# Kernel tuning notes

Measured on AMD Instinct MI355X. Metric: run time of the kernel, lower is better.

## Reference

```python
import jax, jax.numpy as jnp
import numpy as np

N_NODES = 50000
N_EDGES = 800000
H = 64      # node_hidden_size
S = 16      # static_feature_size
EF = 16     # edge_feature_size
ATT_IN = 2 * H + 2 * S + EF   # 176
ATT_W = 2 * H + EF            # 144
UPD_IN = 2 * H                # 128
UPD_W = 2 * H                 # 128


def setup_inputs() -> dict:
    key = jax.random.key(0)
    ks = jax.random.split(key, 12)
    x = jax.random.normal(ks[0], (N_NODES, H), dtype=jnp.float32)
    x_s = jax.random.normal(ks[1], (N_NODES, S), dtype=jnp.float32)
    edge_index = jax.random.randint(ks[2], (2, N_EDGES), 0, N_NODES, dtype=jnp.int32)
    edge_features = jax.random.normal(ks[3], (N_EDGES, EF), dtype=jnp.float32)

    def lin(k, out_dim, in_dim):
        lim = 1.0 / np.sqrt(in_dim)
        kw, kb = jax.random.split(k)
        W = jax.random.uniform(kw, (out_dim, in_dim), minval=-lim, maxval=lim, dtype=jnp.float32)
        b = jax.random.uniform(kb, (out_dim,), minval=-lim, maxval=lim, dtype=jnp.float32)
        return W, b

    att_w1, att_b1 = lin(ks[4], ATT_W, ATT_IN)
    att_w2, att_b2 = lin(ks[5], 1, ATT_W)
    upd_w1, upd_b1 = lin(ks[6], UPD_W, UPD_IN)
    upd_w2, upd_b2 = lin(ks[7], H, UPD_W)

    return {
        "x": x, "x_s": x_s, "edge_index": edge_index, "edge_features": edge_features,
        "att_w1": att_w1, "att_b1": att_b1, "att_w2": att_w2, "att_b2": att_b2,
        "upd_w1": upd_w1, "upd_b1": upd_b1, "upd_w2": upd_w2, "upd_b2": upd_b2,
    }


def segment_softmax(scores, segment_ids, num_segments):
    max_scores = jax.ops.segment_max(scores, segment_ids, num_segments=num_segments)
    exp_scores = jnp.exp(scores - max_scores[segment_ids])
    sum_exp = jax.ops.segment_sum(exp_scores, segment_ids, num_segments=num_segments)
    return exp_scores / (sum_exp[segment_ids] + 1e-9)


def reference(x, x_s, edge_index, edge_features,
              att_w1, att_b1, att_w2, att_b2,
              upd_w1, upd_b1, upd_w2, upd_b2):
    num_nodes = x.shape[0]
    src, dst = edge_index[0], edge_index[1]

    # gather per-edge features: [E, 2H+2S+EF]
    att_in = jnp.concatenate(
        [x[src], x[dst], x_s[src], x_s[dst], edge_features], axis=-1)

    # attention MLP (depth=1, relu hidden), squeeze to [E]
    h = jax.nn.relu(att_in @ att_w1.T + att_b1)
    raw = (h @ att_w2.T + att_b2).squeeze(-1)
    raw = jax.nn.leaky_relu(raw)

    attn = segment_softmax(raw, dst, num_nodes)

    # weighted scatter-sum of source hidden feats -> [N, H]
    aggregated = jax.ops.segment_sum(x[src] * attn[:, None], dst, num_segments=num_nodes)

    upd_in = jnp.concatenate([x, aggregated], axis=-1)
    u = jax.nn.relu(upd_in @ upd_w1.T + upd_b1)
    out = u @ upd_w2.T + upd_b2
    return jax.nn.relu(out)
```

## Files before the change

kernel.cpp:

```cpp
#include <hip/hip_runtime.h>
#include <math.h>

#define N_NODES_C 50000
#define E_C       800000
#define ATT_IN_C  176
#define ATT_HID_C 144
#define SCAN_B    98
#define UPD_TILES 3125
#define DEG_B     3125
#define CVT_B     1978
#define SCORE_B   256

typedef __attribute__((ext_vector_type(8))) __bf16 bf16x8;
typedef __attribute__((ext_vector_type(4))) float f32x4;

#define O_RAW   0L
#define O_DEG   3200000L
#define O_OFF   3400704L
#define O_CUR   3601408L
#define O_CSR   3802112L
#define O_EFC   7002112L
#define O_XB    32602112L
#define O_XSB   39002112L
#define O_W1B   40602112L
#define O_UW1B  40653312L
#define O_UW2B  40686080L
#define O_AGGB  40702464L
#define O_PSUM  O_AGGB

__device__ __forceinline__ bf16x8 bzero8() {
    bf16x8 z;
#pragma unroll
    for (int i = 0; i < 8; ++i) z[i] = (__bf16)0.0f;
    return z;
}

__global__ __launch_bounds__(256) void k_prep(
    const int* __restrict__ ei,
    const float* __restrict__ x, const float* __restrict__ xs,
    const float* __restrict__ w1,
    const float* __restrict__ uw1, const float* __restrict__ uw2,
    int* __restrict__ deg,
    __bf16* __restrict__ xb, __bf16* __restrict__ xsb,
    __bf16* __restrict__ w1b,
    __bf16* __restrict__ uw1b, __bf16* __restrict__ uw2b)
{
    int bid = blockIdx.x;
    if (bid < DEG_B) {
        int e = bid * 256 + threadIdx.x;
        if (e < E_C) atomicAdd(&deg[ei[E_C + e]], 1);
        return;
    }
    long g = (long)(bid - DEG_B) * 256 + threadIdx.x;
    const long G_X = 400000, G_XS = 500000, G_W1 = 503168,
               G_UW1 = 505216, G_UW2 = 506240;
    if (g >= G_UW2) return;
    const float* src; __bf16* dst; long off;
    if (g < G_X)        { src = x;   dst = xb;   off = g * 8; }
    else if (g < G_XS)  { src = xs;  dst = xsb;  off = (g - G_X) * 8; }
    else if (g < G_W1)  { src = w1;  dst = w1b;  off = (g - G_XS) * 8; }
    else if (g < G_UW1) { src = uw1; dst = uw1b; off = (g - G_W1) * 8; }
    else                { src = uw2; dst = uw2b; off = (g - G_UW1) * 8; }
    float4 a = *(const float4*)(src + off);
    float4 b = *(const float4*)(src + off + 4);
    bf16x8 o;
    o[0] = (__bf16)a.x; o[1] = (__bf16)a.y; o[2] = (__bf16)a.z; o[3] = (__bf16)a.w;
    o[4] = (__bf16)b.x; o[5] = (__bf16)b.y; o[6] = (__bf16)b.z; o[7] = (__bf16)b.w;
    *(bf16x8*)(dst + off) = o;
}

__global__ __launch_bounds__(256) void k_scan1(const int* __restrict__ deg,
                                               int* __restrict__ psum) {
    __shared__ int red[256];
    int b = blockIdx.x, t = threadIdx.x;
    int i = b * 512 + t * 2;
    int s = 0;
    if (i < N_NODES_C) s += deg[i];
    if (i + 1 < N_NODES_C) s += deg[i + 1];
    red[t] = s;
    __syncthreads();
#pragma unroll
    for (int off = 128; off > 0; off >>= 1) {
        if (t < off) red[t] += red[t + off];
        __syncthreads();
    }
    if (t == 0) psum[b] = red[0];
}

__global__ __launch_bounds__(256) void k_scan3(const int* __restrict__ deg,
                                               const int* __restrict__ psum,
                                               int* __restrict__ offsets,
                                               int* __restrict__ cursor) {
    __shared__ int sc[256];
    __shared__ int bo[2];
    int b = blockIdx.x, t = threadIdx.x;
    if (t < 64) {
        int v1 = (t < SCAN_B) ? psum[t] : 0;
        int v2 = (t + 64 < SCAN_B) ? psum[t + 64] : 0;
        int c   = ((t < b) ? v1 : 0) + ((t + 64 < b) ? v2 : 0);
        int tot = v1 + v2;
#pragma unroll
        for (int off = 32; off > 0; off >>= 1) {
            c   += __shfl_xor(c, off, 64);
            tot += __shfl_xor(tot, off, 64);
        }
        if (t == 0) { bo[0] = c; bo[1] = tot; }
    }
    int i = b * 512 + t * 2;
    int d0 = (i < N_NODES_C) ? deg[i] : 0;
    int d1 = (i + 1 < N_NODES_C) ? deg[i + 1] : 0;
    int s = d0 + d1;
    sc[t] = s;
    __syncthreads();
#pragma unroll
    for (int off = 1; off < 256; off <<= 1) {
        int val = sc[t];
        int add = (t >= off) ? sc[t - off] : 0;
        __syncthreads();
        sc[t] = val + add;
        __syncthreads();
    }
    int excl = bo[0] + sc[t] - s;
    if (i < N_NODES_C)     { offsets[i]     = excl;      cursor[i]     = excl; }
    if (i + 1 < N_NODES_C) { offsets[i + 1] = excl + d0; cursor[i + 1] = excl + d0; }
    if (b == 0 && t == 0)  offsets[N_NODES_C] = bo[1];
}

__global__ __launch_bounds__(256) void k_fill(const int* __restrict__ ei,
                                              const float* __restrict__ ef,
                                              int* __restrict__ cursor,
                                              unsigned* __restrict__ csrp,
                                              __bf16* __restrict__ efc) {
    int e = blockIdx.x * blockDim.x + threadIdx.x;
    if (e < E_C) {
        int src  = ei[e];
        int dst  = ei[E_C + e];
        int slot = atomicAdd(&cursor[dst], 1);
        csrp[slot] = (unsigned)src | ((unsigned)dst << 16);
        const float4* efp = (const float4*)(ef + (long)e * 16);
        float4 f0 = efp[0], f1 = efp[1], f2 = efp[2], f3 = efp[3];
        bf16x8 o0, o1;
        o0[0] = (__bf16)f0.x; o0[1] = (__bf16)f0.y; o0[2] = (__bf16)f0.z; o0[3] = (__bf16)f0.w;
        o0[4] = (__bf16)f1.x; o0[5] = (__bf16)f1.y; o0[6] = (__bf16)f1.z; o0[7] = (__bf16)f1.w;
        o1[0] = (__bf16)f2.x; o1[1] = (__bf16)f2.y; o1[2] = (__bf16)f2.z; o1[3] = (__bf16)f2.w;
        o1[4] = (__bf16)f3.x; o1[5] = (__bf16)f3.y; o1[6] = (__bf16)f3.z; o1[7] = (__bf16)f3.w;
        __bf16* d = efc + (long)slot * 16;
        *(bf16x8*)d       = o0;
        *(bf16x8*)(d + 8) = o1;
    }
}

__device__ __forceinline__ void load_afrags(
    int src, int dst, long slot, int quad,
    const __bf16* __restrict__ xb, const __bf16* __restrict__ xsb,
    const __bf16* __restrict__ efc,
    bf16x8 a[6])
{
    const __bf16* px = xb + (long)src * 64 + quad * 8;
    const __bf16* pd = xb + (long)dst * 64 + quad * 8;
    a[0] = *(const bf16x8*)(px);
    a[1] = *(const bf16x8*)(px + 32);
    a[2] = *(const bf16x8*)(pd);
    a[3] = *(const bf16x8*)(pd + 32);
    if (quad < 2) {
        a[4] = *(const bf16x8*)(xsb + (long)src * 16 + quad * 8);
        a[5] = *(const bf16x8*)(efc + slot * 16 + quad * 8);
    } else {
        a[4] = *(const bf16x8*)(xsb + (long)dst * 16 + (quad - 2) * 8);
        a[5] = bzero8();
    }
}

__global__ __launch_bounds__(256) void k_scores_mfma(
    const __bf16* __restrict__ xb, const __bf16* __restrict__ xsb,
    const __bf16* __restrict__ efc, const __bf16* __restrict__ w1b,
    const unsigned* __restrict__ csrp,
    const float* __restrict__ b1, const float* __restrict__ w2,
    const float* __restrict__ b2, float* __restrict__ raw)
{
    __shared__ __bf16 w1s[144 * 184];
    int tid  = threadIdx.x;
    int lane = tid & 63;

    for (int c = tid; c < 144 * 22; c += 256) {
        int n = c / 22, kk = (c % 22) * 8;
        *(bf16x8*)&w1s[n * 184 + kk] = *(const bf16x8*)(w1b + (long)n * ATT_IN_C + kk);
    }
    for (int n = tid; n < 144; n += 256)
        *(bf16x8*)&w1s[n * 184 + 176] = bzero8();
    __syncthreads();

    int w = blockIdx.x * 4 + (tid >> 6);
    const int NP = E_C / 32;
    int per = (NP + 1023) / 1024;
    long j0 = (long)w * per;
    long j1 = j0 + per; if (j1 > NP) j1 = NP;
    if (j0 >= j1) return;

    int mrow = lane & 15;
    int quad = lane >> 4;
    const __bf16* wls = &w1s[mrow * 184 + quad * 8];

    float b1v[9], w2v[9];
#pragma unroll
    for (int nt = 0; nt < 9; ++nt) {
        int n = nt * 16 + mrow;
        b1v[nt] = b1[n];
        w2v[nt] = w2[n];
    }
    float b2v = b2[0];

    bf16x8 A0[6], B0[6], A1[6], B1[6];
    {
        unsigned e0 = csrp[j0 * 32 + mrow];
        unsigned e1 = csrp[j0 * 32 + 16 + mrow];
        load_afrags((int)(e0 & 0xFFFFu), (int)(e0 >> 16), j0 * 32 + mrow,
                    quad, xb, xsb, efc, A0);
        load_afrags((int)(e1 & 0xFFFFu), (int)(e1 >> 16), j0 * 32 + 16 + mrow,
                    quad, xb, xsb, efc, B0);
        if (j0 + 1 < j1) {
            unsigned f0 = csrp[(j0 + 1) * 32 + mrow];
            unsigned f1 = csrp[(j0 + 1) * 32 + 16 + mrow];
            load_afrags((int)(f0 & 0xFFFFu), (int)(f0 >> 16), (j0 + 1) * 32 + mrow,
                        quad, xb, xsb, efc, A1);
            load_afrags((int)(f1 & 0xFFFFu), (int)(f1 >> 16), (j0 + 1) * 32 + 16 + mrow,
                        quad, xb, xsb, efc, B1);
        }
    }

    auto body = [&](long j, bf16x8 (&FA)[6], bf16x8 (&FB)[6]) {
        unsigned u0 = 0, u1 = 0;
        bool rl = (j + 2 < j1);
        if (rl) {
            u0 = csrp[(j + 2) * 32 + mrow];
            u1 = csrp[(j + 2) * 32 + 16 + mrow];
        }

        f32x4 accA[9], accB[9];
#pragma unroll
        for (int nt = 0; nt < 9; ++nt) {
            accA[nt] = (f32x4){0.f, 0.f, 0.f, 0.f};
            accB[nt] = (f32x4){0.f, 0.f, 0.f, 0.f};
        }
#pragma unroll
        for (int ks = 0; ks < 6; ++ks) {
#pragma unroll
            for (int nt = 0; nt < 9; ++nt) {
                bf16x8 bf = *(const bf16x8*)(wls + nt * (16 * 184) + ks * 32);
                accA[nt] = __builtin_amdgcn_mfma_f32_16x16x32_bf16(
                    FA[ks], bf, accA[nt], 0, 0, 0);
                accB[nt] = __builtin_amdgcn_mfma_f32_16x16x32_bf16(
                    FB[ks], bf, accB[nt], 0, 0, 0);
            }
        }

        if (rl) {
            load_afrags((int)(u0 & 0xFFFFu), (int)(u0 >> 16), (j + 2) * 32 + mrow,
                        quad, xb, xsb, efc, FA);
            load_afrags((int)(u1 & 0xFFFFu), (int)(u1 >> 16), (j + 2) * 32 + 16 + mrow,
                        quad, xb, xsb, efc, FB);
        }

        float pA0 = 0.f, pA1 = 0.f, pA2 = 0.f, pA3 = 0.f;
        float pB0 = 0.f, pB1 = 0.f, pB2 = 0.f, pB3 = 0.f;
#pragma unroll
        for (int nt = 0; nt < 9; ++nt) {
            pA0 += w2v[nt] * fmaxf(accA[nt][0] + b1v[nt], 0.f);
            pA1 += w2v[nt] * fmaxf(accA[nt][1] + b1v[nt], 0.f);
            pA2 += w2v[nt] * fmaxf(accA[nt][2] + b1v[nt], 0.f);
            pA3 += w2v[nt] * fmaxf(accA[nt][3] + b1v[nt], 0.f);
            pB0 += w2v[nt] * fmaxf(accB[nt][0] + b1v[nt], 0.f);
            pB1 += w2v[nt] * fmaxf(accB[nt][1] + b1v[nt], 0.f);
            pB2 += w2v[nt] * fmaxf(accB[nt][2] + b1v[nt], 0.f);
            pB3 += w2v[nt] * fmaxf(accB[nt][3] + b1v[nt], 0.f);
        }
#pragma unroll
        for (int off = 1; off < 16; off <<= 1) {
            pA0 += __shfl_xor(pA0, off, 64);
            pA1 += __shfl_xor(pA1, off, 64);
            pA2 += __shfl_xor(pA2, off, 64);
            pA3 += __shfl_xor(pA3, off, 64);
            pB0 += __shfl_xor(pB0, off, 64);
            pB1 += __shfl_xor(pB1, off, 64);
            pB2 += __shfl_xor(pB2, off, 64);
            pB3 += __shfl_xor(pB3, off, 64);
        }
        if (mrow < 4) {
            float vA = (mrow == 0) ? pA0 : (mrow == 1) ? pA1 : (mrow == 2) ? pA2 : pA3;
            float vB = (mrow == 0) ? pB0 : (mrow == 1) ? pB1 : (mrow == 2) ? pB2 : pB3;
            vA += b2v; vB += b2v;
            vA = (vA >= 0.f) ? vA : 0.01f * vA;
            vB = (vB >= 0.f) ? vB : 0.01f * vB;
            raw[(j * 2) * 16 + quad * 4 + mrow]     = vA;
            raw[(j * 2 + 1) * 16 + quad * 4 + mrow] = vB;
        }
    };

    long j = j0;
    for (; j + 1 < j1; j += 2) {
        body(j,     A0, B0);
        body(j + 1, A1, B1);
    }
    if (j < j1) body(j, A0, B0);
}

__global__ __launch_bounds__(256) void k_agg(
    const __bf16* __restrict__ xb, const int* __restrict__ offsets,
    const unsigned* __restrict__ csrp,
    const float* __restrict__ raw, __bf16* __restrict__ aggb)
{
    int tid = threadIdx.x;
    int wave = tid >> 6, lane = tid & 63;
    int v = blockIdx.x * 4 + wave;
    if (v >= N_NODES_C) return;
    int s0 = offsets[v], s1 = offsets[v + 1];

    float m = -INFINITY;
    for (int p = s0 + lane; p < s1; p += 64) m = fmaxf(m, raw[p]);
#pragma unroll
    for (int off = 32; off > 0; off >>= 1) m = fmaxf(m, __shfl_xor(m, off, 64));

    float acc = 0.f, sum = 0.f;
    int p = s0;
    for (; p + 4 <= s1; p += 4) {
        unsigned c0 = csrp[p], c1 = csrp[p + 1], c2 = csrp[p + 2], c3 = csrp[p + 3];
        float r0 = raw[p], r1 = raw[p + 1], r2 = raw[p + 2], r3 = raw[p + 3];
        float v0 = (float)xb[(long)(c0 & 0xFFFFu) * 64 + lane];
        float v1 = (float)xb[(long)(c1 & 0xFFFFu) * 64 + lane];
        float v2 = (float)xb[(long)(c2 & 0xFFFFu) * 64 + lane];
        float v3 = (float)xb[(long)(c3 & 0xFFFFu) * 64 + lane];
        float w0 = expf(r0 - m), w1 = expf(r1 - m);
        float w2 = expf(r2 - m), w3 = expf(r3 - m);
        sum += (w0 + w1) + (w2 + w3);
        acc += w0 * v0 + w1 * v1 + w2 * v2 + w3 * v3;
    }
    for (; p < s1; ++p) {
        int src = (int)(csrp[p] & 0xFFFFu);
        float w = expf(raw[p] - m);
        sum += w;
        acc += w * (float)xb[(long)src * 64 + lane];
    }
    aggb[(long)v * 64 + lane] = (__bf16)(acc / (sum + 1e-9f));
}

__global__ __launch_bounds__(256) void k_upd_mfma(
    const __bf16* __restrict__ xb, const __bf16* __restrict__ aggb,
    const __bf16* __restrict__ w1b, const float* __restrict__ b1,
    const __bf16* __restrict__ w2b, const float* __restrict__ b2,
    float* __restrict__ out)
{
    __shared__ __bf16 ubuf[4][16 * 136];
    int tid = threadIdx.x, wid = tid >> 6, lane = tid & 63;
    int tile = blockIdx.x * 4 + wid;
    if (tile >= UPD_TILES) return;
    int mrow = lane & 15, quad = lane >> 4;

    long node = (long)tile * 16 + mrow;
    bf16x8 a1[4];
    a1[0] = *(const bf16x8*)(xb + node * 64 + quad * 8);
    a1[1] = *(const bf16x8*)(xb + node * 64 + 32 + quad * 8);
    a1[2] = *(const bf16x8*)(aggb + node * 64 + quad * 8);
    a1[3] = *(const bf16x8*)(aggb + node * 64 + 32 + quad * 8);

    bf16x8 b1f[4][8];
#pragma unroll
    for (int ks = 0; ks < 4; ++ks)
#pragma unroll
        for (int nt = 0; nt < 8; ++nt)
            b1f[ks][nt] = *(const bf16x8*)(w1b + (long)(nt * 16 + mrow) * 128 + ks * 32 + quad * 8);

    f32x4 acc1[8];
#pragma unroll
    for (int nt = 0; nt < 8; ++nt) acc1[nt] = (f32x4){0.f, 0.f, 0.f, 0.f};
#pragma unroll
    for (int ks = 0; ks < 4; ++ks)
#pragma unroll
        for (int nt = 0; nt < 8; ++nt)
            acc1[nt] = __builtin_amdgcn_mfma_f32_16x16x32_bf16(a1[ks], b1f[ks][nt], acc1[nt], 0, 0, 0);

    __bf16* ub = ubuf[wid];
#pragma unroll
    for (int nt = 0; nt < 8; ++nt) {
        float bb = b1[nt * 16 + mrow];
#pragma unroll
        for (int r = 0; r < 4; ++r) {
            float h = fmaxf(acc1[nt][r] + bb, 0.f);
            ub[(quad * 4 + r) * 136 + nt * 16 + mrow] = (__bf16)h;
        }
    }

    bf16x8 a2[4];
#pragma unroll
    for (int ks = 0; ks < 4; ++ks)
        a2[ks] = *(bf16x8*)&ub[mrow * 136 + ks * 32 + quad * 8];

    bf16x8 b2f[4][4];
#pragma unroll
    for (int ks = 0; ks < 4; ++ks)
#pragma unroll
        for (int nt = 0; nt < 4; ++nt)
            b2f[ks][nt] = *(const bf16x8*)(w2b + (long)(nt * 16 + mrow) * 128 + ks * 32 + quad * 8);

    f32x4 acc2[4];
#pragma unroll
    for (int nt = 0; nt < 4; ++nt) acc2[nt] = (f32x4){0.f, 0.f, 0.f, 0.f};
#pragma unroll
    for (int ks = 0; ks < 4; ++ks)
#pragma unroll
        for (int nt = 0; nt < 4; ++nt)
            acc2[nt] = __builtin_amdgcn_mfma_f32_16x16x32_bf16(a2[ks], b2f[ks][nt], acc2[nt], 0, 0, 0);

#pragma unroll
    for (int nt = 0; nt < 4; ++nt) {
        float bb = b2[nt * 16 + mrow];
#pragma unroll
        for (int r = 0; r < 4; ++r) {
            long nodeo = (long)tile * 16 + quad * 4 + r;
            out[nodeo * 64 + nt * 16 + mrow] = fmaxf(acc2[nt][r] + bb, 0.f);
        }
    }
}

extern "C" void kernel_launch(void* const* d_in, const int* in_sizes, int n_in,
                              void* d_out, int out_size, void* d_ws, size_t ws_size,
                              hipStream_t stream) {
    const float* x    = (const float*)d_in[0];
    const float* xs   = (const float*)d_in[1];
    const int*   ei   = (const int*)d_in[2];
    const float* ef   = (const float*)d_in[3];
    const float* aw1  = (const float*)d_in[4];
    const float* ab1  = (const float*)d_in[5];
    const float* aw2  = (const float*)d_in[6];
    const float* ab2  = (const float*)d_in[7];
    const float* uw1  = (const float*)d_in[8];
    const float* ub1  = (const float*)d_in[9];
    const float* uw2  = (const float*)d_in[10];
    const float* ub2  = (const float*)d_in[11];
    float* out = (float*)d_out;

    char* ws = (char*)d_ws;
    float*     raw     = (float*)(ws + O_RAW);
    int*       deg     = (int*)(ws + O_DEG);
    int*       offsets = (int*)(ws + O_OFF);
    int*       cursor  = (int*)(ws + O_CUR);
    unsigned*  csrp    = (unsigned*)(ws + O_CSR);
    __bf16*    efc     = (__bf16*)(ws + O_EFC);
    __bf16*    xb      = (__bf16*)(ws + O_XB);
    __bf16*    xsb     = (__bf16*)(ws + O_XSB);
    __bf16*    w1b     = (__bf16*)(ws + O_W1B);
    __bf16*    uw1b    = (__bf16*)(ws + O_UW1B);
    __bf16*    uw2b    = (__bf16*)(ws + O_UW2B);
    __bf16*    aggb    = (__bf16*)(ws + O_AGGB);
    int*       psum    = (int*)(ws + O_PSUM);

    hipMemsetAsync(deg, 0, N_NODES_C * sizeof(int), stream);
    hipLaunchKernelGGL(k_prep,     dim3(DEG_B + CVT_B),           dim3(256), 0, stream,
                       ei, x, xs, aw1, uw1, uw2, deg, xb, xsb, w1b, uw1b, uw2b);
    hipLaunchKernelGGL(k_scan1,    dim3(SCAN_B),                  dim3(256), 0, stream, deg, psum);
    hipLaunchKernelGGL(k_scan3,    dim3(SCAN_B),                  dim3(256), 0, stream,
                       deg, psum, offsets, cursor);
    hipLaunchKernelGGL(k_fill,     dim3((E_C + 255) / 256),       dim3(256), 0, stream,
                       ei, ef, cursor, csrp, efc);
    hipLaunchKernelGGL(k_scores_mfma, dim3(SCORE_B),              dim3(256), 0, stream,
                       xb, xsb, efc, w1b, csrp, ab1, aw2, ab2, raw);
    hipLaunchKernelGGL(k_agg,      dim3((N_NODES_C + 3) / 4),     dim3(256), 0, stream,
                       xb, offsets, csrp, raw, aggb);
    hipLaunchKernelGGL(k_upd_mfma, dim3((UPD_TILES + 3) / 4),     dim3(256), 0, stream,
                       xb, aggb, uw1b, ub1, uw2b, ub2, out);
}
```

Before: 336.5 us.

## Fuse softmax aggregation into update MLP kernel and split edge-feature permutation

New measurement: 375.8 us. 11.7% more time.

```diff
diff --git a/kernel.cpp b/kernel.cpp
--- a/kernel.cpp
+++ b/kernel.cpp
@@ -25,8 +25,8 @@
 #define O_W1B   40602112L
 #define O_UW1B  40653312L
 #define O_UW2B  40686080L
-#define O_AGGB  40702464L
-#define O_PSUM  O_AGGB
+#define O_PSUM  40702464L
+#define O_PERM  40703488L
 
 __device__ __forceinline__ bf16x8 bzero8() {
     bf16x8 z;
@@ -127,24 +127,33 @@
 }
 
 __global__ __launch_bounds__(256) void k_fill(const int* __restrict__ ei,
-                                              const float* __restrict__ ef,
                                               int* __restrict__ cursor,
                                               unsigned* __restrict__ csrp,
-                                              __bf16* __restrict__ efc) {
+                                              int* __restrict__ perm) {
     int e = blockIdx.x * blockDim.x + threadIdx.x;
     if (e < E_C) {
         int src  = ei[e];
         int dst  = ei[E_C + e];
         int slot = atomicAdd(&cursor[dst], 1);
         csrp[slot] = (unsigned)src | ((unsigned)dst << 16);
-        const float4* efp = (const float4*)(ef + (long)e * 16);
+        perm[slot] = e;
+    }
+}
+
+__global__ __launch_bounds__(256) void k_fill2(const int* __restrict__ perm,
+                                               const float* __restrict__ ef,
+                                               __bf16* __restrict__ efc) {
+    int s = blockIdx.x * blockDim.x + threadIdx.x;
+    if (s < E_C) {
+        long e = perm[s];
+        const float4* efp = (const float4*)(ef + e * 16);
         float4 f0 = efp[0], f1 = efp[1], f2 = efp[2], f3 = efp[3];
         bf16x8 o0, o1;
         o0[0] = (__bf16)f0.x; o0[1] = (__bf16)f0.y; o0[2] = (__bf16)f0.z; o0[3] = (__bf16)f0.w;
         o0[4] = (__bf16)f1.x; o0[5] = (__bf16)f1.y; o0[6] = (__bf16)f1.z; o0[7] = (__bf16)f1.w;
         o1[0] = (__bf16)f2.x; o1[1] = (__bf16)f2.y; o1[2] = (__bf16)f2.z; o1[3] = (__bf16)f2.w;
         o1[4] = (__bf16)f3.x; o1[5] = (__bf16)f3.y; o1[6] = (__bf16)f3.z; o1[7] = (__bf16)f3.w;
-        __bf16* d = efc + (long)slot * 16;
+        __bf16* d = efc + (long)s * 16;
         *(bf16x8*)d       = o0;
         *(bf16x8*)(d + 8) = o1;
     }
@@ -304,63 +313,57 @@
     if (j < j1) body(j, A0, B0);
 }
 
-__global__ __launch_bounds__(256) void k_agg(
+__global__ __launch_bounds__(256) void k_aggupd(
     const __bf16* __restrict__ xb, const int* __restrict__ offsets,
-    const unsigned* __restrict__ csrp,
-    const float* __restrict__ raw, __bf16* __restrict__ aggb)
-{
-    int tid = threadIdx.x;
-    int wave = tid >> 6, lane = tid & 63;
-    int v = blockIdx.x * 4 + wave;
-    if (v >= N_NODES_C) return;
-    int s0 = offsets[v], s1 = offsets[v + 1];
-
-    float m = -INFINITY;
-    for (int p = s0 + lane; p < s1; p += 64) m = fmaxf(m, raw[p]);
-#pragma unroll
-    for (int off = 32; off > 0; off >>= 1) m = fmaxf(m, __shfl_xor(m, off, 64));
-
-    float acc = 0.f, sum = 0.f;
-    int p = s0;
-    for (; p + 4 <= s1; p += 4) {
-        unsigned c0 = csrp[p], c1 = csrp[p + 1], c2 = csrp[p + 2], c3 = csrp[p + 3];
-        float r0 = raw[p], r1 = raw[p + 1], r2 = raw[p + 2], r3 = raw[p + 3];
-        float v0 = (float)xb[(long)(c0 & 0xFFFFu) * 64 + lane];
-        float v1 = (float)xb[(long)(c1 & 0xFFFFu) * 64 + lane];
-        float v2 = (float)xb[(long)(c2 & 0xFFFFu) * 64 + lane];
-        float v3 = (float)xb[(long)(c3 & 0xFFFFu) * 64 + lane];
-        float w0 = expf(r0 - m), w1 = expf(r1 - m);
-        float w2 = expf(r2 - m), w3 = expf(r3 - m);
-        sum += (w0 + w1) + (w2 + w3);
-        acc += w0 * v0 + w1 * v1 + w2 * v2 + w3 * v3;
-    }
-    for (; p < s1; ++p) {
-        int src = (int)(csrp[p] & 0xFFFFu);
-        float w = expf(raw[p] - m);
-        sum += w;
-        acc += w * (float)xb[(long)src * 64 + lane];
-    }
-    aggb[(long)v * 64 + lane] = (__bf16)(acc / (sum + 1e-9f));
-}
-
-__global__ __launch_bounds__(256) void k_upd_mfma(
-    const __bf16* __restrict__ xb, const __bf16* __restrict__ aggb,
+    const unsigned* __restrict__ csrp, const float* __restrict__ raw,
     const __bf16* __restrict__ w1b, const float* __restrict__ b1,
     const __bf16* __restrict__ w2b, const float* __restrict__ b2,
     float* __restrict__ out)
 {
     __shared__ __bf16 ubuf[4][16 * 136];
+    __shared__ __bf16 aggs[4][16 * 68];
     int tid = threadIdx.x, wid = tid >> 6, lane = tid & 63;
     int tile = blockIdx.x * 4 + wid;
     if (tile >= UPD_TILES) return;
     int mrow = lane & 15, quad = lane >> 4;
 
+    __bf16* ag = aggs[wid];
+    for (int vl = 0; vl < 16; ++vl) {
+        long v = (long)tile * 16 + vl;
+        int s0 = offsets[v], s1 = offsets[v + 1];
+        float m = -INFINITY;
+        for (int p = s0 + lane; p < s1; p += 64) m = fmaxf(m, raw[p]);
+#pragma unroll
+        for (int off = 32; off > 0; off >>= 1) m = fmaxf(m, __shfl_xor(m, off, 64));
+        float acc = 0.f, sum = 0.f;
+        int p = s0;
+        for (; p + 4 <= s1; p += 4) {
+            unsigned c0 = csrp[p], c1 = csrp[p + 1], c2 = csrp[p + 2], c3 = csrp[p + 3];
+            float r0 = raw[p], r1 = raw[p + 1], r2 = raw[p + 2], r3 = raw[p + 3];
+            float v0 = (float)xb[(long)(c0 & 0xFFFFu) * 64 + lane];
+            float v1 = (float)xb[(long)(c1 & 0xFFFFu) * 64 + lane];
+            float v2 = (float)xb[(long)(c2 & 0xFFFFu) * 64 + lane];
+            float v3 = (float)xb[(long)(c3 & 0xFFFFu) * 64 + lane];
+            float w0 = expf(r0 - m), w1 = expf(r1 - m);
+            float w2 = expf(r2 - m), w3 = expf(r3 - m);
+            sum += (w0 + w1) + (w2 + w3);
+            acc += w0 * v0 + w1 * v1 + w2 * v2 + w3 * v3;
+        }
+        for (; p < s1; ++p) {
+            int src = (int)(csrp[p] & 0xFFFFu);
+            float wv = expf(raw[p] - m);
+            sum += wv;
+            acc += wv * (float)xb[(long)src * 64 + lane];
+        }
+        ag[vl * 68 + lane] = (__bf16)(acc / (sum + 1e-9f));
+    }
+
     long node = (long)tile * 16 + mrow;
     bf16x8 a1[4];
     a1[0] = *(const bf16x8*)(xb + node * 64 + quad * 8);
     a1[1] = *(const bf16x8*)(xb + node * 64 + 32 + quad * 8);
-    a1[2] = *(const bf16x8*)(aggb + node * 64 + quad * 8);
-    a1[3] = *(const bf16x8*)(aggb + node * 64 + 32 + quad * 8);
+    a1[2] = *(const bf16x8*)&ag[mrow * 68 + quad * 8];
+    a1[3] = *(const bf16x8*)&ag[mrow * 68 + 32 + quad * 8];
 
     bf16x8 b1f[4][8];
 #pragma unroll
@@ -450,8 +453,8 @@
     __bf16*    w1b     = (__bf16*)(ws + O_W1B);
     __bf16*    uw1b    = (__bf16*)(ws + O_UW1B);
     __bf16*    uw2b    = (__bf16*)(ws + O_UW2B);
-    __bf16*    aggb    = (__bf16*)(ws + O_AGGB);
     int*       psum    = (int*)(ws + O_PSUM);
+    int*       perm    = (int*)(ws + O_PERM);
 
     hipMemsetAsync(deg, 0, N_NODES_C * sizeof(int), stream);
     hipLaunchKernelGGL(k_prep,     dim3(DEG_B + CVT_B),           dim3(256), 0, stream,
@@ -460,11 +463,11 @@
     hipLaunchKernelGGL(k_scan3,    dim3(SCAN_B),                  dim3(256), 0, stream,
                        deg, psum, offsets, cursor);
     hipLaunchKernelGGL(k_fill,     dim3((E_C + 255) / 256),       dim3(256), 0, stream,
-                       ei, ef, cursor, csrp, efc);
+                       ei, cursor, csrp, perm);
+    hipLaunchKernelGGL(k_fill2,    dim3((E_C + 255) / 256),       dim3(256), 0, stream,
+                       perm, ef, efc);
     hipLaunchKernelGGL(k_scores_mfma, dim3(SCORE_B),              dim3(256), 0, stream,
                        xb, xsb, efc, w1b, csrp, ab1, aw2, ab2, raw);
-    hipLaunchKernelGGL(k_agg,      dim3((N_NODES_C + 3) / 4),     dim3(256), 0, stream,
-                       xb, offsets, csrp, raw, aggb);
-    hipLaunchKernelGGL(k_upd_mfma, dim3((UPD_TILES + 3) / 4),     dim3(256), 0, stream,
-                       xb, aggb, uw1b, ub1, uw2b, ub2, out);
-}
+    hipLaunchKernelGGL(k_aggupd,   dim3((UPD_TILES + 3) / 4),     dim3(256), 0, stream,
+                       xb, offsets, csrp, raw, uw1b, ub1, uw2b, ub2, out);
+}
```
